# Kernel optimization log

Hardware: AMD Instinct MI355X
Metric: run time of the kernel (lower is better)

Reference implementation:

```python
import jax, jax.numpy as jnp
import numpy as np

N_NODES = 100000
N_EDGES = 1600000


def _add_self_loops(edge_index, num_nodes):
    loop = jnp.arange(num_nodes, dtype=edge_index.dtype)
    src = jnp.concatenate([edge_index[0], loop])
    dst = jnp.concatenate([edge_index[1], loop])
    return src, dst


def _gcn_conv(x, src, dst, W, b, num_nodes):
    # PyG GCNConv: h = x W, then symmetric-normalized scatter-add aggregation.
    h = x @ W  # [N, F_out]
    ones = jnp.ones(src.shape[0], dtype=x.dtype)
    deg = jax.ops.segment_sum(ones, dst, num_segments=num_nodes)  # in-degree incl. self-loops
    dinv = jnp.where(deg > 0, jax.lax.rsqrt(deg), 0.0)
    norm = dinv[src] * dinv[dst]  # [E]
    msg = h[src] * norm[:, None]  # irregular gather, [E, F_out]
    out = jax.ops.segment_sum(msg, dst, num_segments=num_nodes)  # scatter-add, [N, F_out]
    return out + b


def setup_inputs() -> dict:
    key = jax.random.key(0)
    ks = jax.random.split(key, 4)
    x = jax.random.uniform(ks[0], (N_NODES, 32), dtype=jnp.float32)
    edge_index = jax.random.randint(ks[1], (2, N_EDGES), 0, N_NODES, dtype=jnp.int64)
    W1 = jax.random.normal(ks[2], (32, 64), dtype=jnp.float32) * (1.0 / np.sqrt(32))
    b1 = jnp.zeros((64,), dtype=jnp.float32)
    W2 = jax.random.normal(ks[3], (64, 128), dtype=jnp.float32) * (1.0 / np.sqrt(64))
    b2 = jnp.zeros((128,), dtype=jnp.float32)
    return {"x": x, "edge_index": edge_index, "W1": W1, "b1": b1, "W2": W2, "b2": b2}


def reference(x, edge_index, W1, b1, W2, b2):
    num_nodes = x.shape[0]
    src, dst = _add_self_loops(edge_index, num_nodes)
    h = _gcn_conv(x, src, dst, W1, b1, num_nodes)
    h = jax.nn.relu(h)
    out = _gcn_conv(h, src, dst, W2, b2, num_nodes)
    return out
```

## Files before the change

kernel.cpp:

```cpp
#include <hip/hip_runtime.h>
#include <hip/hip_fp16.h>

static inline int cdiv(int a, int b) { return (a + b - 1) / b; }

#define NWORD 25600
#define HC    64
#define NPART 8
#define SUB   256

struct h2x4 { __half2 a, b, c, d; };

__global__ __launch_bounds__(1024) void k_hist(const int* __restrict__ dst, int E, int N, int chunk,
                                               unsigned char* __restrict__ rank8,
                                               unsigned char* __restrict__ Mb) {
    __shared__ unsigned int cnt[NWORD];
    int c = blockIdx.x;
    for (int i = threadIdx.x; i < NWORD; i += 1024) cnt[i] = 0;
    __syncthreads();
    int ebeg = c * chunk;
    int eend = min(E, ebeg + chunk);
    for (int e = ebeg + threadIdx.x; e < eend; e += 1024) {
        int d = dst[e];
        int sh = (d & 3) * 8;
        unsigned int old = atomicAdd(&cnt[d >> 2], 1u << sh);
        rank8[e] = (unsigned char)((old >> sh) & 0xFF);
    }
    __syncthreads();
    unsigned int* Mrow = (unsigned int*)(Mb + (size_t)c * N);
    int nw = N >> 2;
    for (int i = threadIdx.x; i < nw; i += 1024) Mrow[i] = cnt[i];
}

__global__ __launch_bounds__(256) void k_degpre(const unsigned char* __restrict__ Mb, int N,
                                                unsigned char* __restrict__ pre8,
                                                int* __restrict__ deg, float* __restrict__ dinv) {
    int i = blockIdx.x * 256 + threadIdx.x;
    if (i >= (N >> 2)) return;
    unsigned int s0 = 0, s1 = 0, s2 = 0, s3 = 0;
#pragma unroll
    for (int c = 0; c < HC; ++c) {
        unsigned int w = *(const unsigned int*)(Mb + (size_t)c * N + 4 * i);
        *(unsigned int*)(pre8 + (size_t)c * N + 4 * i) = s0 | (s1 << 8) | (s2 << 16) | (s3 << 24);
        s0 += w & 0xFF; s1 += (w >> 8) & 0xFF; s2 += (w >> 16) & 0xFF; s3 += (w >> 24) & 0xFF;
    }
    ((int4*)deg)[i] = make_int4((int)s0, (int)s1, (int)s2, (int)s3);
    ((float4*)dinv)[i] = make_float4(rsqrtf((float)(s0 + 1)), rsqrtf((float)(s1 + 1)),
                                     rsqrtf((float)(s2 + 1)), rsqrtf((float)(s3 + 1)));
}

#define SCAN_BS 1024

__global__ __launch_bounds__(SCAN_BS) void k_blocksum(const int* __restrict__ deg, int N, int* __restrict__ bsum) {
    __shared__ int s[SCAN_BS];
    int t = threadIdx.x;
    int i = blockIdx.x * SCAN_BS + t;
    s[t] = (i < N) ? deg[i] : 0;
    __syncthreads();
    for (int off = SCAN_BS / 2; off > 0; off >>= 1) {
        if (t < off) s[t] += s[t + off];
        __syncthreads();
    }
    if (t == 0) bsum[blockIdx.x] = s[0];
}

__global__ __launch_bounds__(128) void k_scan_bsums(const int* __restrict__ bsum, int NB, int* __restrict__ boff) {
    __shared__ int s[128];
    int t = threadIdx.x;
    int v = (t < NB) ? bsum[t] : 0;
    s[t] = v;
    __syncthreads();
    for (int off = 1; off < 128; off <<= 1) {
        int u = (t >= off) ? s[t - off] : 0;
        __syncthreads();
        s[t] += u;
        __syncthreads();
    }
    if (t < NB) boff[t] = s[t] - v;
}

__global__ __launch_bounds__(SCAN_BS) void k_scan_final(const int* __restrict__ deg, int N,
                                                        const int* __restrict__ boff,
                                                        int* __restrict__ offsets, int E) {
    __shared__ int s[SCAN_BS];
    int t = threadIdx.x;
    int i = blockIdx.x * SCAN_BS + t;
    int v = (i < N) ? deg[i] : 0;
    s[t] = v;
    __syncthreads();
    for (int off = 1; off < SCAN_BS; off <<= 1) {
        int u = (t >= off) ? s[t - off] : 0;
        __syncthreads();
        s[t] += u;
        __syncthreads();
    }
    if (i < N) offsets[i] = boff[blockIdx.x] + s[t] - v;
    if (blockIdx.x == 0 && t == 0) offsets[N] = E;
}

__global__ __launch_bounds__(256) void k_scatter_part(const int* __restrict__ ei, int E, int N, int chunk,
                                                      int espb, int part,
                                                      const int* __restrict__ offsets,
                                                      const unsigned char* __restrict__ pre8,
                                                      const unsigned char* __restrict__ rank8,
                                                      int* __restrict__ csr_src) {
    int p = blockIdx.x & (NPART - 1);
    int sub = blockIdx.x >> 3;
    int lo = p * part;
    int hi = min(N, lo + part);
    int beg = sub * espb;
    int end = min(E, beg + espb);
    const int* dst = ei + E;
    for (int e = beg + threadIdx.x; e < end; e += 256) {
        int d = dst[e];
        if (d >= lo && d < hi) {
            int c = e / chunk;
            int pos = offsets[d] + (int)pre8[(size_t)c * N + d] + (int)rank8[e];
            csr_src[pos] = ei[e];
        }
    }
}

__global__ __launch_bounds__(256) void k_cast32(const float* __restrict__ x, const float* __restrict__ dinv,
                                                __half* __restrict__ xh, int N) {
    int i = blockIdx.x * 256 + threadIdx.x;
    if (i >= N * 8) return;
    int g = i >> 3;
    float di = dinv[g];
    float4 v = ((const float4*)x)[i];
    __half2 h0 = __floats2half2_rn(v.x * di, v.y * di);
    __half2 h1 = __floats2half2_rn(v.z * di, v.w * di);
    ((__half2*)xh)[2 * i] = h0;
    ((__half2*)xh)[2 * i + 1] = h1;
}

template <int F>
__global__ __launch_bounds__(256) void k_agg(const __half* __restrict__ feat,
                                             const int* __restrict__ offsets,
                                             const int* __restrict__ csr_src,
                                             const float* __restrict__ dinv,
                                             float* __restrict__ out, int N) {
    constexpr int L = F / 8;
    int t = blockIdx.x * 256 + threadIdx.x;
    int g = t / L;
    int q = t % L;
    if (g >= N) return;
    const h2x4* f8 = (const h2x4*)feat;
    int beg = offsets[g];
    int end = offsets[g + 1];
    float di = dinv[g];
    float acc[8];
    {
        h2x4 w = f8[(size_t)g * L + q];
        float2 p0 = __half22float2(w.a), p1 = __half22float2(w.b);
        float2 p2 = __half22float2(w.c), p3 = __half22float2(w.d);
        acc[0] = p0.x; acc[1] = p0.y; acc[2] = p1.x; acc[3] = p1.y;
        acc[4] = p2.x; acc[5] = p2.y; acc[6] = p3.x; acc[7] = p3.y;
    }
    int e = beg;
    for (; e + 4 <= end; e += 4) {
        int s0 = csr_src[e + 0], s1 = csr_src[e + 1], s2 = csr_src[e + 2], s3 = csr_src[e + 3];
        h2x4 w0 = f8[(size_t)s0 * L + q];
        h2x4 w1 = f8[(size_t)s1 * L + q];
        h2x4 w2 = f8[(size_t)s2 * L + q];
        h2x4 w3 = f8[(size_t)s3 * L + q];
        float2 u;
        u = __half22float2(w0.a); acc[0] += u.x; acc[1] += u.y;
        u = __half22float2(w0.b); acc[2] += u.x; acc[3] += u.y;
        u = __half22float2(w0.c); acc[4] += u.x; acc[5] += u.y;
        u = __half22float2(w0.d); acc[6] += u.x; acc[7] += u.y;
        u = __half22float2(w1.a); acc[0] += u.x; acc[1] += u.y;
        u = __half22float2(w1.b); acc[2] += u.x; acc[3] += u.y;
        u = __half22float2(w1.c); acc[4] += u.x; acc[5] += u.y;
        u = __half22float2(w1.d); acc[6] += u.x; acc[7] += u.y;
        u = __half22float2(w2.a); acc[0] += u.x; acc[1] += u.y;
        u = __half22float2(w2.b); acc[2] += u.x; acc[3] += u.y;
        u = __half22float2(w2.c); acc[4] += u.x; acc[5] += u.y;
        u = __half22float2(w2.d); acc[6] += u.x; acc[7] += u.y;
        u = __half22float2(w3.a); acc[0] += u.x; acc[1] += u.y;
        u = __half22float2(w3.b); acc[2] += u.x; acc[3] += u.y;
        u = __half22float2(w3.c); acc[4] += u.x; acc[5] += u.y;
        u = __half22float2(w3.d); acc[6] += u.x; acc[7] += u.y;
    }
    for (; e < end; ++e) {
        h2x4 w = f8[(size_t)csr_src[e] * L + q];
        float2 u;
        u = __half22float2(w.a); acc[0] += u.x; acc[1] += u.y;
        u = __half22float2(w.b); acc[2] += u.x; acc[3] += u.y;
        u = __half22float2(w.c); acc[4] += u.x; acc[5] += u.y;
        u = __half22float2(w.d); acc[6] += u.x; acc[7] += u.y;
    }
    float4 o0 = make_float4(acc[0] * di, acc[1] * di, acc[2] * di, acc[3] * di);
    float4 o1 = make_float4(acc[4] * di, acc[5] * di, acc[6] * di, acc[7] * di);
    ((float4*)out)[(size_t)g * (F / 4) + q * 2] = o0;
    ((float4*)out)[(size_t)g * (F / 4) + q * 2 + 1] = o1;
}

__global__ __launch_bounds__(256) void k_gemm1(const float* __restrict__ A, const float* __restrict__ W,
                                               const float* __restrict__ b, const float* __restrict__ dinv,
                                               __half* __restrict__ out, int N) {
    __shared__ float sA[32][68];
    __shared__ float sW[32][64];
    int tid = threadIdx.x;
    int row0 = blockIdx.x * 64;

    {
        const float4* Wv = (const float4*)W;
        float4* sWv = (float4*)&sW[0][0];
        sWv[tid] = Wv[tid];
        sWv[tid + 256] = Wv[tid + 256];
    }
    {
        int row = tid >> 2;
        int gr = row0 + row;
        int kq = (tid & 3) * 4;
#pragma unroll
        for (int i = 0; i < 2; ++i) {
            int k0 = kq + 16 * i;
            float4 v = (gr < N) ? *(const float4*)(A + (size_t)gr * 32 + k0)
                                : make_float4(0.f, 0.f, 0.f, 0.f);
            sA[k0 + 0][row] = v.x;
            sA[k0 + 1][row] = v.y;
            sA[k0 + 2][row] = v.z;
            sA[k0 + 3][row] = v.w;
        }
    }
    __syncthreads();

    int tm = tid & 15, tn = tid >> 4;
    float acc[4][4];
#pragma unroll
    for (int i = 0; i < 4; ++i) {
        float4 bb = *(const float4*)(b + tn * 4);
        acc[i][0] = bb.x; acc[i][1] = bb.y; acc[i][2] = bb.z; acc[i][3] = bb.w;
    }
#pragma unroll 4
    for (int k = 0; k < 32; ++k) {
        float4 a = *(const float4*)&sA[k][tm * 4];
        float4 w = *(const float4*)&sW[k][tn * 4];
        float av[4] = {a.x, a.y, a.z, a.w};
        float wv[4] = {w.x, w.y, w.z, w.w};
#pragma unroll
        for (int i = 0; i < 4; ++i)
#pragma unroll
            for (int j = 0; j < 4; ++j) acc[i][j] = fmaf(av[i], wv[j], acc[i][j]);
    }
#pragma unroll
    for (int i = 0; i < 4; ++i) {
        int row = row0 + tm * 4 + i;
        if (row < N) {
            float di = dinv[row];
            __half2 p0 = __floats2half2_rn(fmaxf(acc[i][0], 0.f) * di, fmaxf(acc[i][1], 0.f) * di);
            __half2 p1 = __floats2half2_rn(fmaxf(acc[i][2], 0.f) * di, fmaxf(acc[i][3], 0.f) * di);
            __half2* op = (__half2*)(out + (size_t)row * 64);
            op[tn * 2] = p0;
            op[tn * 2 + 1] = p1;
        }
    }
}

__global__ __launch_bounds__(256) void k_gemm2(const float* __restrict__ A, const float* __restrict__ W,
                                               const float* __restrict__ b, float* __restrict__ out, int N) {
    __shared__ float sA[64][68];
    __shared__ float sW[64][128];
    int tid = threadIdx.x;
    int row0 = blockIdx.x * 64;

    {
        const float4* Wv = (const float4*)W;
        float4* sWv = (float4*)&sW[0][0];
#pragma unroll
        for (int i = 0; i < 8; ++i) sWv[tid + 256 * i] = Wv[tid + 256 * i];
    }
    {
        int row = tid >> 2;
        int gr = row0 + row;
        int kq = (tid & 3) * 4;
#pragma unroll
        for (int i = 0; i < 4; ++i) {
            int k0 = kq + 16 * i;
            float4 v = (gr < N) ? *(const float4*)(A + (size_t)gr * 64 + k0)
                                : make_float4(0.f, 0.f, 0.f, 0.f);
            sA[k0 + 0][row] = v.x;
            sA[k0 + 1][row] = v.y;
            sA[k0 + 2][row] = v.z;
            sA[k0 + 3][row] = v.w;
        }
    }
    __syncthreads();

    int tm = tid & 15, tn = tid >> 4;
    float acc[4][8];
    {
        float4 b0 = *(const float4*)(b + tn * 8);
        float4 b1 = *(const float4*)(b + tn * 8 + 4);
#pragma unroll
        for (int i = 0; i < 4; ++i) {
            acc[i][0] = b0.x; acc[i][1] = b0.y; acc[i][2] = b0.z; acc[i][3] = b0.w;
            acc[i][4] = b1.x; acc[i][5] = b1.y; acc[i][6] = b1.z; acc[i][7] = b1.w;
        }
    }
#pragma unroll 4
    for (int k = 0; k < 64; ++k) {
        float4 a = *(const float4*)&sA[k][tm * 4];
        float4 w0 = *(const float4*)&sW[k][tn * 8];
        float4 w1 = *(const float4*)&sW[k][tn * 8 + 4];
        float av[4] = {a.x, a.y, a.z, a.w};
        float wv[8] = {w0.x, w0.y, w0.z, w0.w, w1.x, w1.y, w1.z, w1.w};
#pragma unroll
        for (int i = 0; i < 4; ++i)
#pragma unroll
            for (int j = 0; j < 8; ++j) acc[i][j] = fmaf(av[i], wv[j], acc[i][j]);
    }
#pragma unroll
    for (int i = 0; i < 4; ++i) {
        int row = row0 + tm * 4 + i;
        if (row < N) {
            *(float4*)(out + (size_t)row * 128 + tn * 8) =
                make_float4(acc[i][0], acc[i][1], acc[i][2], acc[i][3]);
            *(float4*)(out + (size_t)row * 128 + tn * 8 + 4) =
                make_float4(acc[i][4], acc[i][5], acc[i][6], acc[i][7]);
        }
    }
}

extern "C" void kernel_launch(void* const* d_in, const int* in_sizes, int n_in,
                              void* d_out, int out_size, void* d_ws, size_t ws_size,
                              hipStream_t stream) {
    const float* x  = (const float*)d_in[0];
    const int*   ei = (const int*)d_in[1];
    const float* W1 = (const float*)d_in[2];
    const float* b1 = (const float*)d_in[3];
    const float* W2 = (const float*)d_in[4];
    const float* b2 = (const float*)d_in[5];
    float* out = (float*)d_out;

    const int N = in_sizes[0] / 32;
    const int E = in_sizes[1] / 2;
    const int chunk = cdiv(E, HC);
    const int espb = cdiv(E, SUB);
    const int part = cdiv(N, NPART);

    char* ws = (char*)d_ws;
    size_t off = 0;
    auto walloc = [&](size_t bytes) -> void* {
        void* p = ws + off;
        off = (off + bytes + 255) & ~(size_t)255;
        return p;
    };
    unsigned char* Mb      = (unsigned char*) walloc((size_t)HC * N);
    unsigned char* pre8    = (unsigned char*) walloc((size_t)HC * N);
    int*           deg     = (int*)           walloc((size_t)N * 4);
    float*         dinv    = (float*)         walloc((size_t)N * 4);
    int*           offsets = (int*)           walloc((size_t)(N + 4) * 4);
    int*           bsum    = (int*)           walloc(128 * 4);
    int*           boff    = (int*)           walloc(128 * 4);
    unsigned char* rank8   = (unsigned char*) walloc((size_t)E);
    int*           csr_src = (int*)           walloc((size_t)E * 4);
    __half*        xh      = (__half*)        walloc((size_t)N * 32 * 2);
    float*         a1      = (float*)         walloc((size_t)N * 32 * 4);
    __half*        h2h     = (__half*)        walloc((size_t)N * 64 * 2);
    float*         a2      = (float*)         walloc((size_t)N * 64 * 4);
    (void)ws_size; (void)n_in; (void)out_size;

    k_hist<<<HC, 1024, 0, stream>>>(ei + E, E, N, chunk, rank8, Mb);
    k_degpre<<<cdiv(N / 4, 256), 256, 0, stream>>>(Mb, N, pre8, deg, dinv);

    const int NB = cdiv(N, SCAN_BS);
    k_blocksum<<<NB, SCAN_BS, 0, stream>>>(deg, N, bsum);
    k_scan_bsums<<<1, 128, 0, stream>>>(bsum, NB, boff);
    k_scan_final<<<NB, SCAN_BS, 0, stream>>>(deg, N, boff, offsets, E);

    k_cast32<<<cdiv(N * 8, 256), 256, 0, stream>>>(x, dinv, xh, N);
    k_scatter_part<<<NPART * SUB, 256, 0, stream>>>(ei, E, N, chunk, espb, part,
                                                    offsets, pre8, rank8, csr_src);

    k_agg<32><<<cdiv(N * 4, 256), 256, 0, stream>>>(xh, offsets, csr_src, dinv, a1, N);
    k_gemm1<<<cdiv(N, 64), 256, 0, stream>>>(a1, W1, b1, dinv, h2h, N);

    k_agg<64><<<cdiv(N * 8, 256), 256, 0, stream>>>(h2h, offsets, csr_src, dinv, a2, N);
    k_gemm2<<<cdiv(N, 64), 256, 0, stream>>>(a2, W2, b2, out, N);
}
```

Baseline: 167.3 us.

## Replace partitioned CSR scatter with cooperative bucketed two-pass scatter

The old pass read the destination array eight times, once per node partition, and wrote source indices straight to random CSR positions. The new version uses one cooperative kernel over 256 blocks. Each block computes every edge's CSR position once and histograms positions into 4096-slot buckets. A grid-wide scan then lets each edge be written as a packed (source, in-bucket offset) word into a bucket-contiguous staging array. A second kernel scatters each bucket inside shared memory and writes contiguous CSR rows, replacing random global writes with local ones at the cost of extra passes, several grid syncs, and a staging buffer. Packing the source into 17 bits assumes node ids fit below 131072, and MAXK=7 assumes each block gets at most 7168 edges.

```diff
diff --git a/kernel.cpp b/kernel.cpp
--- a/kernel.cpp
+++ b/kernel.cpp
@@ -1,12 +1,18 @@
 #include <hip/hip_runtime.h>
 #include <hip/hip_fp16.h>
+#include <hip/hip_cooperative_groups.h>
+
+namespace cg = cooperative_groups;
 
 static inline int cdiv(int a, int b) { return (a + b - 1) / b; }
 
 #define NWORD 25600
 #define HC    64
-#define NPART 8
-#define SUB   256
+#define NBLK  256
+#define CTHR  1024
+#define MAXK  7
+#define BKT_SHIFT 12
+#define BKT   (1 << BKT_SHIFT)
 
 struct h2x4 { __half2 a, b, c, d; };
 
@@ -97,27 +103,108 @@
     if (blockIdx.x == 0 && t == 0) offsets[N] = E;
 }
 
-__global__ __launch_bounds__(256) void k_scatter_part(const int* __restrict__ ei, int E, int N, int chunk,
-                                                      int espb, int part,
-                                                      const int* __restrict__ offsets,
-                                                      const unsigned char* __restrict__ pre8,
-                                                      const unsigned char* __restrict__ rank8,
-                                                      int* __restrict__ csr_src) {
-    int p = blockIdx.x & (NPART - 1);
-    int sub = blockIdx.x >> 3;
-    int lo = p * part;
-    int hi = min(N, lo + part);
-    int beg = sub * espb;
-    int end = min(E, beg + espb);
+__global__ __launch_bounds__(CTHR) void k_sortcsr(const int* __restrict__ ei, int E, int N, int chunk,
+                                                  int epb, int nbuk, int clen,
+                                                  const int* __restrict__ offsets,
+                                                  const unsigned char* __restrict__ pre8,
+                                                  const unsigned char* __restrict__ rank8,
+                                                  int* __restrict__ cnt, int* __restrict__ bsum2,
+                                                  int* __restrict__ boff2, int* __restrict__ cbase,
+                                                  unsigned int* __restrict__ pairs) {
+    cg::grid_group grid = cg::this_grid();
+    __shared__ int h[512];
+    __shared__ int s[CTHR];
+    int blk = blockIdx.x, tid = threadIdx.x;
+    for (int b = tid; b < nbuk; b += CTHR) h[b] = 0;
+    __syncthreads();
+    int beg = blk * epb;
+    int end = min(E, beg + epb);
     const int* dst = ei + E;
-    for (int e = beg + threadIdx.x; e < end; e += 256) {
-        int d = dst[e];
-        if (d >= lo && d < hi) {
-            int c = e / chunk;
+    int c0 = beg / chunk;
+    int bound = (c0 + 1) * chunk;
+    int ps[MAXK], sr[MAXK];
+#pragma unroll
+    for (int k = 0; k < MAXK; ++k) {
+        int e = beg + tid + k * CTHR;
+        ps[k] = -1;
+        if (e < end) {
+            int d = dst[e];
+            int c = (e < bound) ? c0 : c0 + 1;
             int pos = offsets[d] + (int)pre8[(size_t)c * N + d] + (int)rank8[e];
-            csr_src[pos] = ei[e];
-        }
-    }
+            ps[k] = pos;
+            sr[k] = ei[e];
+            atomicAdd(&h[pos >> BKT_SHIFT], 1);
+        }
+    }
+    __syncthreads();
+    for (int b = tid; b < nbuk; b += CTHR) cnt[b * NBLK + blk] = h[b];
+    grid.sync();
+    int NB2 = (clen + CTHR - 1) / CTHR;
+    if (blk < NB2) {
+        int i = blk * CTHR + tid;
+        s[tid] = (i < clen) ? cnt[i] : 0;
+        __syncthreads();
+        for (int off = CTHR / 2; off > 0; off >>= 1) {
+            if (tid < off) s[tid] += s[tid + off];
+            __syncthreads();
+        }
+        if (tid == 0) bsum2[blk] = s[0];
+    }
+    grid.sync();
+    if (blk == 0) {
+        int v = (tid < NB2) ? bsum2[tid] : 0;
+        s[tid] = v;
+        __syncthreads();
+        for (int off = 1; off < CTHR; off <<= 1) {
+            int u = (tid >= off) ? s[tid - off] : 0;
+            __syncthreads();
+            s[tid] += u;
+            __syncthreads();
+        }
+        if (tid < NB2) boff2[tid] = s[tid] - v;
+    }
+    grid.sync();
+    if (blk < NB2) {
+        int i = blk * CTHR + tid;
+        int v = (i < clen) ? cnt[i] : 0;
+        s[tid] = v;
+        __syncthreads();
+        for (int off = 1; off < CTHR; off <<= 1) {
+            int u = (tid >= off) ? s[tid - off] : 0;
+            __syncthreads();
+            s[tid] += u;
+            __syncthreads();
+        }
+        if (i < clen) cbase[i] = boff2[blk] + s[tid] - v;
+    }
+    grid.sync();
+    for (int b = tid; b < nbuk; b += CTHR) h[b] = cbase[b * NBLK + blk];
+    __syncthreads();
+#pragma unroll
+    for (int k = 0; k < MAXK; ++k) {
+        if (ps[k] >= 0) {
+            int slot = atomicAdd(&h[ps[k] >> BKT_SHIFT], 1);
+            pairs[slot] = (unsigned)sr[k] | ((unsigned)(ps[k] & (BKT - 1)) << 17);
+        }
+    }
+}
+
+__global__ __launch_bounds__(1024) void k_scat2(const unsigned int* __restrict__ pairs, int E,
+                                                int* __restrict__ csr) {
+    __shared__ int buf[BKT];
+    int b = blockIdx.x;
+    int base = b << BKT_SHIFT;
+    int n = min(BKT, E - base);
+    for (int i = threadIdx.x; i < n; i += 1024) {
+        unsigned int p = pairs[base + i];
+        buf[p >> 17] = (int)(p & 0x1FFFFu);
+    }
+    __syncthreads();
+    int n4 = n >> 2;
+    for (int i = threadIdx.x; i < n4; i += 1024)
+        ((int4*)(csr + base))[i] = ((const int4*)buf)[i];
+    for (int i = (n4 << 2) + threadIdx.x; i < n; i += 1024)
+        csr[base + i] = buf[i];
 }
 
 __global__ __launch_bounds__(256) void k_cast32(const float* __restrict__ x, const float* __restrict__ dinv,
@@ -337,8 +424,9 @@
     const int N = in_sizes[0] / 32;
     const int E = in_sizes[1] / 2;
     const int chunk = cdiv(E, HC);
-    const int espb = cdiv(E, SUB);
-    const int part = cdiv(N, NPART);
+    const int epb = cdiv(E, NBLK);
+    const int nbuk = cdiv(E, BKT);
+    const int clen = nbuk * NBLK;
 
     char* ws = (char*)d_ws;
     size_t off = 0;
@@ -355,6 +443,11 @@
     int*           bsum    = (int*)           walloc(128 * 4);
     int*           boff    = (int*)           walloc(128 * 4);
     unsigned char* rank8   = (unsigned char*) walloc((size_t)E);
+    int*           cnt     = (int*)           walloc((size_t)(clen + 4) * 4);
+    int*           bsum2   = (int*)           walloc(1024 * 4);
+    int*           boff2   = (int*)           walloc(1024 * 4);
+    int*           cbase   = (int*)           walloc((size_t)(clen + 4) * 4);
+    unsigned int*  pairs   = (unsigned int*)  walloc((size_t)E * 4);
     int*           csr_src = (int*)           walloc((size_t)E * 4);
     __half*        xh      = (__half*)        walloc((size_t)N * 32 * 2);
     float*         a1      = (float*)         walloc((size_t)N * 32 * 4);
@@ -371,8 +464,19 @@
     k_scan_final<<<NB, SCAN_BS, 0, stream>>>(deg, N, boff, offsets, E);
 
     k_cast32<<<cdiv(N * 8, 256), 256, 0, stream>>>(x, dinv, xh, N);
-    k_scatter_part<<<NPART * SUB, 256, 0, stream>>>(ei, E, N, chunk, espb, part,
-                                                    offsets, pre8, rank8, csr_src);
+
+    {
+        const int* ei_ = ei; int E_ = E, N_ = N, chunk_ = chunk, epb_ = epb, nbuk_ = nbuk, clen_ = clen;
+        const int* offsets_ = offsets;
+        const unsigned char* pre8_ = pre8;
+        const unsigned char* rank8_ = rank8;
+        int* cnt_ = cnt; int* bsum2_ = bsum2; int* boff2_ = boff2; int* cbase_ = cbase;
+        unsigned int* pairs_ = pairs;
+        void* args[] = {&ei_, &E_, &N_, &chunk_, &epb_, &nbuk_, &clen_,
+                        &offsets_, &pre8_, &rank8_, &cnt_, &bsum2_, &boff2_, &cbase_, &pairs_};
+        hipLaunchCooperativeKernel((const void*)k_sortcsr, dim3(NBLK), dim3(CTHR), args, 0, stream);
+    }
+    k_scat2<<<nbuk, 1024, 0, stream>>>(pairs, E, csr_src);
 
     k_agg<32><<<cdiv(N * 4, 256), 256, 0, stream>>>(xh, offsets, csr_src, dinv, a1, N);
     k_gemm1<<<cdiv(N, 64), 256, 0, stream>>>(a1, W1, b1, dinv, h2h, N);
```

After: 292.5 us. +74.8%, slower.

## Replace per-chunk byte histograms with two-level bucket sort for CSR build

Applied to the files above, without the earlier changes.

The CSR construction moves from 64 per-chunk byte histograms over all nodes, followed by a partitioned scatter, to a two-pass bucket sort. Edges are first counted and placed into 256-node buckets with per-block shared-memory atomics, then each bucket is sorted locally in shared memory, which also produces offsets and dinv. This removes the large HC*N byte matrices and the 8x redundant rescans of the edge list. In exchange it assumes src fits in 17 bits, at most 6144 edges per bucket and at most 512 buckets, and these limits hold only for this input size and distribution.

```diff
diff --git a/kernel.cpp b/kernel.cpp
--- a/kernel.cpp
+++ b/kernel.cpp
@@ -3,58 +3,31 @@
 
 static inline int cdiv(int a, int b) { return (a + b - 1) / b; }
 
-#define NWORD 25600
-#define HC    64
-#define NPART 8
-#define SUB   256
+#define BK_SHIFT 8
+#define NBLK2 1024
+#define SCAN_BS 1024
+#define MAXB 6144
 
 struct h2x4 { __half2 a, b, c, d; };
 
-__global__ __launch_bounds__(1024) void k_hist(const int* __restrict__ dst, int E, int N, int chunk,
-                                               unsigned char* __restrict__ rank8,
-                                               unsigned char* __restrict__ Mb) {
-    __shared__ unsigned int cnt[NWORD];
-    int c = blockIdx.x;
-    for (int i = threadIdx.x; i < NWORD; i += 1024) cnt[i] = 0;
-    __syncthreads();
-    int ebeg = c * chunk;
-    int eend = min(E, ebeg + chunk);
-    for (int e = ebeg + threadIdx.x; e < eend; e += 1024) {
-        int d = dst[e];
-        int sh = (d & 3) * 8;
-        unsigned int old = atomicAdd(&cnt[d >> 2], 1u << sh);
-        rank8[e] = (unsigned char)((old >> sh) & 0xFF);
-    }
-    __syncthreads();
-    unsigned int* Mrow = (unsigned int*)(Mb + (size_t)c * N);
-    int nw = N >> 2;
-    for (int i = threadIdx.x; i < nw; i += 1024) Mrow[i] = cnt[i];
-}
-
-__global__ __launch_bounds__(256) void k_degpre(const unsigned char* __restrict__ Mb, int N,
-                                                unsigned char* __restrict__ pre8,
-                                                int* __restrict__ deg, float* __restrict__ dinv) {
-    int i = blockIdx.x * 256 + threadIdx.x;
-    if (i >= (N >> 2)) return;
-    unsigned int s0 = 0, s1 = 0, s2 = 0, s3 = 0;
-#pragma unroll
-    for (int c = 0; c < HC; ++c) {
-        unsigned int w = *(const unsigned int*)(Mb + (size_t)c * N + 4 * i);
-        *(unsigned int*)(pre8 + (size_t)c * N + 4 * i) = s0 | (s1 << 8) | (s2 << 16) | (s3 << 24);
-        s0 += w & 0xFF; s1 += (w >> 8) & 0xFF; s2 += (w >> 16) & 0xFF; s3 += (w >> 24) & 0xFF;
-    }
-    ((int4*)deg)[i] = make_int4((int)s0, (int)s1, (int)s2, (int)s3);
-    ((float4*)dinv)[i] = make_float4(rsqrtf((float)(s0 + 1)), rsqrtf((float)(s1 + 1)),
-                                     rsqrtf((float)(s2 + 1)), rsqrtf((float)(s3 + 1)));
-}
-
-#define SCAN_BS 1024
-
-__global__ __launch_bounds__(SCAN_BS) void k_blocksum(const int* __restrict__ deg, int N, int* __restrict__ bsum) {
+__global__ __launch_bounds__(256) void kb1(const int* __restrict__ dst, int E, int epb, int nbuk,
+                                           int* __restrict__ cnt) {
+    __shared__ int h[512];
+    int blk = blockIdx.x;
+    for (int b = threadIdx.x; b < nbuk; b += 256) h[b] = 0;
+    __syncthreads();
+    int beg = blk * epb, end = min(E, beg + epb);
+    for (int e = beg + threadIdx.x; e < end; e += 256)
+        atomicAdd(&h[dst[e] >> BK_SHIFT], 1);
+    __syncthreads();
+    for (int b = threadIdx.x; b < nbuk; b += 256) cnt[(size_t)b * NBLK2 + blk] = h[b];
+}
+
+__global__ __launch_bounds__(SCAN_BS) void k_blocksum(const int* __restrict__ v, int n, int* __restrict__ bsum) {
     __shared__ int s[SCAN_BS];
     int t = threadIdx.x;
     int i = blockIdx.x * SCAN_BS + t;
-    s[t] = (i < N) ? deg[i] : 0;
+    s[t] = (i < n) ? v[i] : 0;
     __syncthreads();
     for (int off = SCAN_BS / 2; off > 0; off >>= 1) {
         if (t < off) s[t] += s[t + off];
@@ -63,13 +36,13 @@
     if (t == 0) bsum[blockIdx.x] = s[0];
 }
 
-__global__ __launch_bounds__(128) void k_scan_bsums(const int* __restrict__ bsum, int NB, int* __restrict__ boff) {
-    __shared__ int s[128];
+__global__ __launch_bounds__(512) void k_scan_bsums(const int* __restrict__ bsum, int NB, int* __restrict__ boff) {
+    __shared__ int s[512];
     int t = threadIdx.x;
     int v = (t < NB) ? bsum[t] : 0;
     s[t] = v;
     __syncthreads();
-    for (int off = 1; off < 128; off <<= 1) {
+    for (int off = 1; off < 512; off <<= 1) {
         int u = (t >= off) ? s[t - off] : 0;
         __syncthreads();
         s[t] += u;
@@ -78,14 +51,14 @@
     if (t < NB) boff[t] = s[t] - v;
 }
 
-__global__ __launch_bounds__(SCAN_BS) void k_scan_final(const int* __restrict__ deg, int N,
+__global__ __launch_bounds__(SCAN_BS) void k_scan_final(const int* __restrict__ v, int n,
                                                         const int* __restrict__ boff,
-                                                        int* __restrict__ offsets, int E) {
+                                                        int* __restrict__ outp, int E) {
     __shared__ int s[SCAN_BS];
     int t = threadIdx.x;
     int i = blockIdx.x * SCAN_BS + t;
-    int v = (i < N) ? deg[i] : 0;
-    s[t] = v;
+    int x = (i < n) ? v[i] : 0;
+    s[t] = x;
     __syncthreads();
     for (int off = 1; off < SCAN_BS; off <<= 1) {
         int u = (t >= off) ? s[t - off] : 0;
@@ -93,31 +66,79 @@
         s[t] += u;
         __syncthreads();
     }
-    if (i < N) offsets[i] = boff[blockIdx.x] + s[t] - v;
-    if (blockIdx.x == 0 && t == 0) offsets[N] = E;
-}
-
-__global__ __launch_bounds__(256) void k_scatter_part(const int* __restrict__ ei, int E, int N, int chunk,
-                                                      int espb, int part,
-                                                      const int* __restrict__ offsets,
-                                                      const unsigned char* __restrict__ pre8,
-                                                      const unsigned char* __restrict__ rank8,
-                                                      int* __restrict__ csr_src) {
-    int p = blockIdx.x & (NPART - 1);
-    int sub = blockIdx.x >> 3;
-    int lo = p * part;
-    int hi = min(N, lo + part);
-    int beg = sub * espb;
-    int end = min(E, beg + espb);
+    if (i < n) outp[i] = boff[blockIdx.x] + s[t] - x;
+    if (blockIdx.x == 0 && t == 0) outp[n] = E;
+}
+
+__global__ __launch_bounds__(256) void kb2(const int* __restrict__ ei, int E, int epb, int nbuk,
+                                           const int* __restrict__ cbase,
+                                           unsigned int* __restrict__ pairs) {
+    __shared__ int lb[512];
+    int blk = blockIdx.x;
+    for (int b = threadIdx.x; b < nbuk; b += 256) lb[b] = cbase[(size_t)b * NBLK2 + blk];
+    __syncthreads();
+    int beg = blk * epb, end = min(E, beg + epb);
     const int* dst = ei + E;
     for (int e = beg + threadIdx.x; e < end; e += 256) {
         int d = dst[e];
-        if (d >= lo && d < hi) {
-            int c = e / chunk;
-            int pos = offsets[d] + (int)pre8[(size_t)c * N + d] + (int)rank8[e];
-            csr_src[pos] = ei[e];
-        }
-    }
+        int s = ei[e];
+        int slot = atomicAdd(&lb[d >> BK_SHIFT], 1);
+        pairs[slot] = (unsigned)s | ((unsigned)(d & 255) << 17);
+    }
+}
+
+__global__ __launch_bounds__(1024) void k_sortbucket(const unsigned int* __restrict__ pairs,
+                                                     const int* __restrict__ cbase, int nbuk, int N, int E,
+                                                     int* __restrict__ csr_src,
+                                                     int* __restrict__ offsets,
+                                                     float* __restrict__ dinv) {
+    __shared__ int c[256];
+    __shared__ int ex[256];
+    __shared__ int sorted[MAXB];
+    int b = blockIdx.x;
+    int tid = threadIdx.x;
+    int base = cbase[(size_t)b * NBLK2];
+    int endp = cbase[(size_t)(b + 1) * NBLK2];
+    int n = endp - base;
+    if (tid < 256) c[tid] = 0;
+    __syncthreads();
+    int sr_[6], dl_[6], rk_[6];
+#pragma unroll
+    for (int k = 0; k < 6; ++k) {
+        int i = tid + k * 1024;
+        if (i < n) {
+            unsigned int p = pairs[base + i];
+            sr_[k] = (int)(p & 0x1FFFFu);
+            dl_[k] = (int)(p >> 17);
+            rk_[k] = atomicAdd(&c[dl_[k]], 1);
+        }
+    }
+    __syncthreads();
+    if (tid < 256) ex[tid] = c[tid];
+    __syncthreads();
+    for (int off = 1; off < 256; off <<= 1) {
+        int u = (tid >= off && tid < 256) ? ex[tid - off] : 0;
+        __syncthreads();
+        if (tid < 256) ex[tid] += u;
+        __syncthreads();
+    }
+    if (tid < 256) ex[tid] -= c[tid];
+    __syncthreads();
+#pragma unroll
+    for (int k = 0; k < 6; ++k) {
+        int i = tid + k * 1024;
+        if (i < n) sorted[ex[dl_[k]] + rk_[k]] = sr_[k];
+    }
+    __syncthreads();
+    for (int i = tid; i < n; i += 1024) csr_src[base + i] = sorted[i];
+    if (tid < 256) {
+        int g = (b << BK_SHIFT) + tid;
+        if (g < N) {
+            offsets[g] = base + ex[tid];
+            dinv[g] = rsqrtf((float)(c[tid] + 1));
+        }
+    }
+    if (b == 0 && tid == 0) offsets[N] = E;
 }
 
 __global__ __launch_bounds__(256) void k_cast32(const float* __restrict__ x, const float* __restrict__ dinv,
@@ -336,9 +357,9 @@
 
     const int N = in_sizes[0] / 32;
     const int E = in_sizes[1] / 2;
-    const int chunk = cdiv(E, HC);
-    const int espb = cdiv(E, SUB);
-    const int part = cdiv(N, NPART);
+    const int epb = cdiv(E, NBLK2);
+    const int nbuk = cdiv(N, 1 << BK_SHIFT);
+    const int clen = nbuk * NBLK2;
 
     char* ws = (char*)d_ws;
     size_t off = 0;
@@ -347,32 +368,31 @@
         off = (off + bytes + 255) & ~(size_t)255;
         return p;
     };
-    unsigned char* Mb      = (unsigned char*) walloc((size_t)HC * N);
-    unsigned char* pre8    = (unsigned char*) walloc((size_t)HC * N);
-    int*           deg     = (int*)           walloc((size_t)N * 4);
-    float*         dinv    = (float*)         walloc((size_t)N * 4);
-    int*           offsets = (int*)           walloc((size_t)(N + 4) * 4);
-    int*           bsum    = (int*)           walloc(128 * 4);
-    int*           boff    = (int*)           walloc(128 * 4);
-    unsigned char* rank8   = (unsigned char*) walloc((size_t)E);
-    int*           csr_src = (int*)           walloc((size_t)E * 4);
-    __half*        xh      = (__half*)        walloc((size_t)N * 32 * 2);
-    float*         a1      = (float*)         walloc((size_t)N * 32 * 4);
-    __half*        h2h     = (__half*)        walloc((size_t)N * 64 * 2);
-    float*         a2      = (float*)         walloc((size_t)N * 64 * 4);
+    int*          cnt     = (int*)          walloc((size_t)(clen + 4) * 4);
+    int*          cbase   = (int*)          walloc((size_t)(clen + 4) * 4);
+    int*          bsum    = (int*)          walloc(512 * 4);
+    int*          boff    = (int*)          walloc(512 * 4);
+    unsigned int* pairs   = (unsigned int*) walloc((size_t)E * 4);
+    int*          csr_src = (int*)          walloc((size_t)E * 4);
+    int*          offsets = (int*)          walloc((size_t)(N + 4) * 4);
+    float*        dinv    = (float*)        walloc((size_t)N * 4);
+    __half*       xh      = (__half*)       walloc((size_t)N * 32 * 2);
+    float*        a1      = (float*)        walloc((size_t)N * 32 * 4);
+    __half*       h2h     = (__half*)       walloc((size_t)N * 64 * 2);
+    float*        a2      = (float*)        walloc((size_t)N * 64 * 4);
     (void)ws_size; (void)n_in; (void)out_size;
 
-    k_hist<<<HC, 1024, 0, stream>>>(ei + E, E, N, chunk, rank8, Mb);
-    k_degpre<<<cdiv(N / 4, 256), 256, 0, stream>>>(Mb, N, pre8, deg, dinv);
-
-    const int NB = cdiv(N, SCAN_BS);
-    k_blocksum<<<NB, SCAN_BS, 0, stream>>>(deg, N, bsum);
-    k_scan_bsums<<<1, 128, 0, stream>>>(bsum, NB, boff);
-    k_scan_final<<<NB, SCAN_BS, 0, stream>>>(deg, N, boff, offsets, E);
+    kb1<<<NBLK2, 256, 0, stream>>>(ei + E, E, epb, nbuk, cnt);
+
+    const int NB = cdiv(clen, SCAN_BS);
+    k_blocksum<<<NB, SCAN_BS, 0, stream>>>(cnt, clen, bsum);
+    k_scan_bsums<<<1, 512, 0, stream>>>(bsum, NB, boff);
+    k_scan_final<<<NB, SCAN_BS, 0, stream>>>(cnt, clen, boff, cbase, E);
+
+    kb2<<<NBLK2, 256, 0, stream>>>(ei, E, epb, nbuk, cbase, pairs);
+    k_sortbucket<<<nbuk, 1024, 0, stream>>>(pairs, cbase, nbuk, N, E, csr_src, offsets, dinv);
 
     k_cast32<<<cdiv(N * 8, 256), 256, 0, stream>>>(x, dinv, xh, N);
-    k_scatter_part<<<NPART * SUB, 256, 0, stream>>>(ei, E, N, chunk, espb, part,
-                                                    offsets, pre8, rank8, csr_src);
 
     k_agg<32><<<cdiv(N * 4, 256), 256, 0, stream>>>(xh, offsets, csr_src, dinv, a1, N);
     k_gemm1<<<cdiv(N, 64), 256, 0, stream>>>(a1, W1, b1, dinv, h2h, N);
```

New measurement: 151.6 us. 9.4% less time.
